# Optimization experiments

Measured on AMD Instinct MI355X. Metric: run time of the kernel, lower is better.

Reference implementation:

```python
import jax, jax.numpy as jnp
import numpy as np

D_MODEL = 1024
NUM_ATOMS = 16384
TEMPERATURE = 1.0
NEG_INF = -1e9


def setup_inputs() -> dict:
    key = jax.random.key(0)
    kx, kd, km = jax.random.split(key, 3)
    x = jax.random.normal(kx, (4, 2048, D_MODEL), dtype=jnp.float32)
    # xavier_uniform for [num_atoms, d_model]
    limit = float(np.sqrt(6.0 / (NUM_ATOMS + D_MODEL)))
    dictionary = jax.random.uniform(
        kd, (NUM_ATOMS, D_MODEL), dtype=jnp.float32, minval=-limit, maxval=limit
    )
    mask = jax.random.randint(km, (4, 2048, NUM_ATOMS), 0, 2, dtype=jnp.int32)
    return {"x": x, "dictionary": dictionary, "mask": mask}


def reference(x, dictionary, mask):
    # scores: [b, s, num_atoms]
    scores = jnp.einsum("bsd,ad->bsa", x, dictionary)
    m = mask.astype(scores.dtype)
    scores = scores * m + (1.0 - m) * NEG_INF
    weights = jax.nn.softmax(scores / TEMPERATURE, axis=-1)
    reconstruction = jnp.einsum("bsa,ad->bsd", weights, dictionary)
    argmax_indices = jnp.argmax(scores, axis=-1)
    return reconstruction, argmax_indices
```

## Files before the change

### kernel.cpp

```cpp
#include <hip/hip_runtime.h>

#define NTOK   8192
#define DMODEL 1024
#define NATOM  16384

typedef _Float16 half8  __attribute__((ext_vector_type(8)));
typedef _Float16 half4_t __attribute__((ext_vector_type(4)));
typedef float    f32x4  __attribute__((ext_vector_type(4)));

#define GLOAD_LDS16(gsrc, ldst) \
  __builtin_amdgcn_global_load_lds((const __attribute__((address_space(1))) unsigned int*)(gsrc), \
                                   (__attribute__((address_space(3))) unsigned int*)(ldst), 16, 0, 0)

__global__ void cvt_f32_f16(const float* __restrict__ in, _Float16* __restrict__ out, int n4) {
  int i = blockIdx.x * 256 + threadIdx.x;
  if (i >= n4) return;
  float4 v = ((const float4*)in)[i];
  half4_t h;
  h[0] = (_Float16)v.x; h[1] = (_Float16)v.y; h[2] = (_Float16)v.z; h[3] = (_Float16)v.w;
  ((half4_t*)out)[i] = h;
}

__global__ void transpose_dict(const float* __restrict__ dict,
                               _Float16* __restrict__ Dh, _Float16* __restrict__ dT) {
  __shared__ _Float16 tile[64][68];
  int a0 = blockIdx.x * 64;
  int d0 = blockIdx.y * 64;
  int tid = threadIdx.x;
  int c = tid & 63;
  int r0 = tid >> 6;
  #pragma unroll
  for (int i = 0; i < 16; i++) {
    int r = r0 + i * 4;
    _Float16 h = (_Float16)dict[(size_t)(a0 + r) * DMODEL + d0 + c];
    tile[r][c] = h;
    Dh[(size_t)(a0 + r) * DMODEL + d0 + c] = h;
  }
  __syncthreads();
  #pragma unroll
  for (int i = 0; i < 16; i++) {
    int rd = r0 + i * 4;
    dT[(size_t)(d0 + rd) * NATOM + a0 + c] = tile[c][rd];
  }
}

__global__ void zero_lsum(float* __restrict__ lsum) {
  lsum[blockIdx.x * 256 + threadIdx.x] = 0.0f;
}

__device__ __forceinline__ void stage_ab(const _Float16* __restrict__ A,
                                         const _Float16* __restrict__ B,
                                         _Float16* As, _Float16* Bs,
                                         size_t arow0, size_t brow0, size_t ldk,
                                         int k0, int tid) {
  #pragma unroll
  for (int i = 0; i < 2; i++) {
    int L = tid + i * 256;
    int r = L >> 2, pc = L & 3;
    int c = pc ^ ((r >> 1) & 3);
    GLOAD_LDS16(A + (arow0 + r) * ldk + k0 + c * 8, As + (size_t)L * 8);
    GLOAD_LDS16(B + (brow0 + r) * ldk + k0 + c * 8, Bs + (size_t)L * 8);
  }
}

__device__ __forceinline__ void stage_item(const _Float16* __restrict__ src, int row0,
                                           int kt, int s, _Float16* dst, int tid) {
  #pragma unroll
  for (int i = 0; i < 2; i++) {
    int L2 = tid + i * 512;
    int r = L2 >> 2, q = L2 & 3;
    int c = s * 4 + (q ^ ((r >> 1) & 3));
    GLOAD_LDS16(src + (size_t)(row0 + r) * DMODEL + kt * 64 + c * 8, dst + (size_t)L2 * 8);
  }
}

__launch_bounds__(512, 2)
__global__ void score_kernel(const _Float16* __restrict__ Xh,
                             const _Float16* __restrict__ Dh,
                             const int* __restrict__ mask,
                             _Float16* __restrict__ E,
                             float* __restrict__ lsum,
                             _Float16* __restrict__ Tmax) {
  __shared__ _Float16 lds[65536];
  const int tid  = threadIdx.x;
  const int lane = tid & 63;
  const int wave = tid >> 6;
  const int wm = wave >> 2;
  const int wn = wave & 3;
  const int m0 = blockIdx.y * 256;
  const int n0 = blockIdx.x * 256;

  const int frow = lane & 15;
  const int fkc  = lane >> 4;

  f32x4 acc[8][4] = {};

  #define AOFF(B_, S_, ROW_) ((B_) * 32768 + (S_) * 8192 + (((ROW_) << 2) + (fkc ^ (((ROW_) >> 1) & 3))) * 8)
  #define BOFF(B_, S_, ROW_) ((B_) * 32768 + 16384 + (S_) * 8192 + (((ROW_) << 2) + (fkc ^ (((ROW_) >> 1) & 3))) * 8)

  stage_item(Xh, m0, 0, 0, lds,         tid);
  stage_item(Dh, n0, 0, 0, lds + 16384, tid);
  stage_item(Xh, m0, 0, 1, lds + 8192,  tid);
  stage_item(Dh, n0, 0, 1, lds + 24576, tid);
  asm volatile("s_waitcnt vmcnt(4)" ::: "memory");
  __builtin_amdgcn_s_barrier();

  const int NKT = DMODEL / 64;
  for (int kt = 0; kt < NKT; ++kt) {
    const int b  = kt & 1;
    const int nb = b ^ 1;
    const bool more = (kt + 1 < NKT);
    half8 af[4], bf[4];

    #pragma unroll
    for (int i = 0; i < 4; i++) af[i] = *(const half8*)&lds[AOFF(b, 0, wm * 128 + i * 16 + frow)];
    #pragma unroll
    for (int j = 0; j < 4; j++) bf[j] = *(const half8*)&lds[BOFF(b, 0, wn * 64 + j * 16 + frow)];
    if (more) stage_item(Xh, m0, kt + 1, 0, lds + nb * 32768, tid);
    asm volatile("s_waitcnt lgkmcnt(0)" ::: "memory");
    __builtin_amdgcn_sched_barrier(0);
    __builtin_amdgcn_s_setprio(1);
    #pragma unroll
    for (int i = 0; i < 4; i++)
      #pragma unroll
      for (int j = 0; j < 4; j++)
        acc[i][j] = __builtin_amdgcn_mfma_f32_16x16x32_f16(af[i], bf[j], acc[i][j], 0, 0, 0);
    __builtin_amdgcn_s_setprio(0);
    __builtin_amdgcn_sched_barrier(0);
    __builtin_amdgcn_s_barrier();

    #pragma unroll
    for (int i = 0; i < 4; i++) af[i] = *(const half8*)&lds[AOFF(b, 0, wm * 128 + 64 + i * 16 + frow)];
    if (more) stage_item(Dh, n0, kt + 1, 0, lds + nb * 32768 + 16384, tid);
    asm volatile("s_waitcnt lgkmcnt(0)" ::: "memory");
    __builtin_amdgcn_sched_barrier(0);
    __builtin_amdgcn_s_setprio(1);
    #pragma unroll
    for (int i = 0; i < 4; i++)
      #pragma unroll
      for (int j = 0; j < 4; j++)
        acc[4 + i][j] = __builtin_amdgcn_mfma_f32_16x16x32_f16(af[i], bf[j], acc[4 + i][j], 0, 0, 0);
    __builtin_amdgcn_s_setprio(0);
    __builtin_amdgcn_sched_barrier(0);
    if (more) asm volatile("s_waitcnt vmcnt(4)" ::: "memory");
    else      asm volatile("s_waitcnt vmcnt(0)" ::: "memory");
    __builtin_amdgcn_s_barrier();

    #pragma unroll
    for (int i = 0; i < 4; i++) af[i] = *(const half8*)&lds[AOFF(b, 1, wm * 128 + i * 16 + frow)];
    #pragma unroll
    for (int j = 0; j < 4; j++) bf[j] = *(const half8*)&lds[BOFF(b, 1, wn * 64 + j * 16 + frow)];
    if (more) stage_item(Xh, m0, kt + 1, 1, lds + nb * 32768 + 8192, tid);
    asm volatile("s_waitcnt lgkmcnt(0)" ::: "memory");
    __builtin_amdgcn_sched_barrier(0);
    __builtin_amdgcn_s_setprio(1);
    #pragma unroll
    for (int i = 0; i < 4; i++)
      #pragma unroll
      for (int j = 0; j < 4; j++)
        acc[i][j] = __builtin_amdgcn_mfma_f32_16x16x32_f16(af[i], bf[j], acc[i][j], 0, 0, 0);
    __builtin_amdgcn_s_setprio(0);
    __builtin_amdgcn_sched_barrier(0);
    __builtin_amdgcn_s_barrier();

    #pragma unroll
    for (int i = 0; i < 4; i++) af[i] = *(const half8*)&lds[AOFF(b, 1, wm * 128 + 64 + i * 16 + frow)];
    if (more) stage_item(Dh, n0, kt + 1, 1, lds + nb * 32768 + 24576, tid);
    asm volatile("s_waitcnt lgkmcnt(0)" ::: "memory");
    __builtin_amdgcn_sched_barrier(0);
    __builtin_amdgcn_s_setprio(1);
    #pragma unroll
    for (int i = 0; i < 4; i++)
      #pragma unroll
      for (int j = 0; j < 4; j++)
        acc[4 + i][j] = __builtin_amdgcn_mfma_f32_16x16x32_f16(af[i], bf[j], acc[4 + i][j], 0, 0, 0);
    __builtin_amdgcn_s_setprio(0);
    __builtin_amdgcn_sched_barrier(0);
    if (more) asm volatile("s_waitcnt vmcnt(4)" ::: "memory");
    __builtin_amdgcn_s_barrier();
  }
  #undef AOFF
  #undef BOFF

  const int cr = (lane >> 4) * 4;
  const int cc = lane & 15;
  #pragma unroll
  for (int h = 0; h < 2; h++) {
    if ((wn >> 1) == h) {
      #pragma unroll
      for (int i = 0; i < 8; i++) {
        #pragma unroll
        for (int j = 0; j < 4; j++) {
          #pragma unroll
          for (int r = 0; r < 4; r++) {
            int lr = wm * 128 + i * 16 + cr + r;
            int lc = (wn & 1) * 64 + j * 16 + cc;
            lds[lr * 136 + lc] = (_Float16)__expf(acc[i][j][r]);
          }
        }
      }
    }
    __builtin_amdgcn_s_barrier();
    #pragma unroll
    for (int i = 0; i < 8; i++) {
      int chunk = i * 512 + tid;
      int r  = chunk >> 4;
      int c8 = (chunk & 15) * 8;
      half8 v = *(const half8*)&lds[r * 136 + c8];
      const int* mp = &mask[(size_t)(m0 + r) * NATOM + n0 + h * 128 + c8];
      int4 k0 = *(const int4*)mp;
      int4 k1 = *(const int4*)(mp + 4);
      half8 e;
      e[0] = k0.x ? v[0] : (_Float16)0.0f;
      e[1] = k0.y ? v[1] : (_Float16)0.0f;
      e[2] = k0.z ? v[2] : (_Float16)0.0f;
      e[3] = k0.w ? v[3] : (_Float16)0.0f;
      e[4] = k1.x ? v[4] : (_Float16)0.0f;
      e[5] = k1.y ? v[5] : (_Float16)0.0f;
      e[6] = k1.z ? v[6] : (_Float16)0.0f;
      e[7] = k1.w ? v[7] : (_Float16)0.0f;
      *(half8*)&E[(size_t)(m0 + r) * NATOM + n0 + h * 128 + c8] = e;
      float s = 0.0f, m = 0.0f;
      #pragma unroll
      for (int j = 0; j < 8; j++) { float f = (float)e[j]; s += f; m = fmaxf(m, f); }
      s += __shfl_xor(s, 1, 64); m = fmaxf(m, __shfl_xor(m, 1, 64));
      s += __shfl_xor(s, 2, 64); m = fmaxf(m, __shfl_xor(m, 2, 64));
      s += __shfl_xor(s, 4, 64); m = fmaxf(m, __shfl_xor(m, 4, 64));
      s += __shfl_xor(s, 8, 64); m = fmaxf(m, __shfl_xor(m, 8, 64));
      if ((tid & 15) == 0) {
        atomicAdd(&lsum[m0 + r], s);
        Tmax[(size_t)(m0 + r) * 128 + blockIdx.x * 2 + h] = (_Float16)m;
      }
    }
    __builtin_amdgcn_s_barrier();
  }
}

__global__ void scan_lite(const _Float16* __restrict__ E,
                          const _Float16* __restrict__ Tmax,
                          const float* __restrict__ x,
                          const float* __restrict__ dict,
                          float* __restrict__ argout) {
  const int wv   = threadIdx.x >> 6;
  const int lane = threadIdx.x & 63;
  const int t = blockIdx.x * 4 + wv;

  __shared__ int    cnt[4];
  __shared__ int    cand[4][32];
  __shared__ double csc[4][32];
  if (lane == 0) cnt[wv] = 0;

  const _Float16* tm = Tmax + (size_t)t * 128;
  float m0 = (float)tm[lane];
  float m1 = (float)tm[64 + lane];
  float mx = fmaxf(m0, m1);
  #pragma unroll
  for (int off = 32; off > 0; off >>= 1) mx = fmaxf(mx, __shfl_xor(mx, off, 64));

  if (mx > 0.0f) {
    float thr = 0.98f * mx;
    unsigned long long q0 = __ballot(m0 >= thr);
    unsigned long long q1 = __ballot(m1 >= thr);
    while (q0 | q1) {
      int tile;
      if (q0) { tile = __ffsll(q0) - 1; q0 &= q0 - 1; }
      else    { tile = 64 + __ffsll(q1) - 1; q1 &= q1 - 1; }
      const _Float16* ep = E + (size_t)t * NATOM + tile * 128;
      float e0 = (float)ep[lane], e1 = (float)ep[64 + lane];
      if (e0 >= thr) { int p = atomicAdd(&cnt[wv], 1); if (p < 32) cand[wv][p] = tile * 128 + lane; }
      if (e1 >= thr) { int p = atomicAdd(&cnt[wv], 1); if (p < 32) cand[wv][p] = tile * 128 + 64 + lane; }
    }
  }
  int nc = min(cnt[wv], 32);
  const float* xr = x + (size_t)t * DMODEL;
  for (int c = 0; c < nc; c++) {
    const float* dr = dict + (size_t)cand[wv][c] * DMODEL;
    double a = 0.0;
    #pragma unroll
    for (int i = 0; i < 16; i++) {
      int d = lane + i * 64;
      a += (double)xr[d] * (double)dr[d];
    }
    #pragma unroll
    for (int off = 32; off > 0; off >>= 1) a += __shfl_down(a, off, 64);
    if (lane == 0) csc[wv][c] = a;
  }
  if (lane == 0) {
    int best = 0;
    if (nc > 0) {
      double bs = -1e300;
      best = NATOM;
      for (int c = 0; c < nc; c++)
        if (csc[wv][c] > bs || (csc[wv][c] == bs && cand[wv][c] < best)) { bs = csc[wv][c]; best = cand[wv][c]; }
    }
    argout[t] = (float)best;
  }
}

__launch_bounds__(256, 2)
__global__ void recon_kernel(const _Float16* __restrict__ E,
                             const _Float16* __restrict__ DT,
                             const float* __restrict__ lsum,
                             float* __restrict__ out) {
  __shared__ _Float16 lds[32768];
  const int tid  = threadIdx.x;
  const int lane = tid & 63;
  const int wave = tid >> 6;
  const int wm = wave >> 1, wn = wave & 1;
  const int swz = (blockIdx.x & 7) * 64 + (blockIdx.x >> 3);
  const int n0 = (swz & 7) * 128;
  const int m0 = (swz >> 3) * 128;

  const int frow = lane & 15;
  const int fkc  = lane >> 4;

  f32x4 acc[4][4] = {};

  stage_ab(E, DT, lds,         lds + 4096,  m0, n0, NATOM, 0,  tid);
  stage_ab(E, DT, lds + 8192,  lds + 12288, m0, n0, NATOM, 32, tid);
  stage_ab(E, DT, lds + 16384, lds + 20480, m0, n0, NATOM, 64, tid);

  for (int t = 0; t < 512; ++t) {
    if (t < 510)       asm volatile("s_waitcnt vmcnt(8)" ::: "memory");
    else if (t == 510) asm volatile("s_waitcnt vmcnt(4)" ::: "memory");
    else               asm volatile("s_waitcnt vmcnt(0)" ::: "memory");
    __builtin_amdgcn_s_barrier();
    __builtin_amdgcn_sched_barrier(0);
    const _Float16* As = lds + (t & 3) * 8192;
    const _Float16* Bs = As + 4096;
    half8 af[4], bf[4];
    #pragma unroll
    for (int i = 0; i < 4; i++) {
      int ar = wm * 64 + i * 16 + frow;
      int br = wn * 64 + i * 16 + frow;
      af[i] = *(const half8*)&As[ar * 32 + ((fkc ^ ((ar >> 1) & 3)) << 3)];
      bf[i] = *(const half8*)&Bs[br * 32 + ((fkc ^ ((br >> 1) & 3)) << 3)];
    }
    if (t + 3 < 512) {
      int b = (t + 3) & 3;
      stage_ab(E, DT, lds + b * 8192, lds + b * 8192 + 4096, m0, n0, NATOM, (t + 3) * 32, tid);
    }
    __builtin_amdgcn_s_setprio(1);
    #pragma unroll
    for (int i = 0; i < 4; i++)
      #pragma unroll
      for (int j = 0; j < 4; j++)
        acc[i][j] = __builtin_amdgcn_mfma_f32_16x16x32_f16(af[i], bf[j], acc[i][j], 0, 0, 0);
    __builtin_amdgcn_s_setprio(0);
    __builtin_amdgcn_sched_barrier(0);
  }

  const int cr = (lane >> 4) * 4;
  const int cc = lane & 15;
  #pragma unroll
  for (int i = 0; i < 4; i++) {
    #pragma unroll
    for (int r = 0; r < 4; r++) {
      int lr = wm * 64 + i * 16 + cr + r;
      float sc = 1.0f / lsum[m0 + lr];
      #pragma unroll
      for (int j = 0; j < 4; j++) {
        int lc = wn * 64 + j * 16 + cc;
        out[(size_t)(m0 + lr) * DMODEL + (n0 + lc)] = acc[i][j][r] * sc;
      }
    }
  }
}

extern "C" void kernel_launch(void* const* d_in, const int* in_sizes, int n_in,
                              void* d_out, int out_size, void* d_ws, size_t ws_size,
                              hipStream_t stream) {
  const float* x    = (const float*)d_in[0];
  const float* dict = (const float*)d_in[1];
  const int*   mask = (const int*)d_in[2];
  float* recon  = (float*)d_out;
  float* argout = recon + (size_t)NTOK * DMODEL;

  char* w = (char*)d_ws;
  _Float16* Xh = (_Float16*)(w);
  _Float16* Dh = (_Float16*)(w + (size_t)16  * 1024 * 1024);
  _Float16* DT = (_Float16*)(w + (size_t)48  * 1024 * 1024);
  _Float16* E  = (_Float16*)(w + (size_t)80  * 1024 * 1024);
  float*  lsum = (float*)  (w + (size_t)336 * 1024 * 1024);
  _Float16* Tmax = (_Float16*)d_out;

  cvt_f32_f16<<<dim3(NTOK * DMODEL / 4 / 256), 256, 0, stream>>>(x, Xh, NTOK * DMODEL / 4);
  transpose_dict<<<dim3(NATOM / 64, DMODEL / 64), 256, 0, stream>>>(dict, Dh, DT);
  zero_lsum<<<dim3(NTOK / 256), 256, 0, stream>>>(lsum);
  score_kernel<<<dim3(NATOM / 256, NTOK / 256), 512, 0, stream>>>(Xh, Dh, mask, E, lsum, Tmax);
  scan_lite<<<dim3(NTOK / 4), 256, 0, stream>>>(E, Tmax, x, dict, argout);
  recon_kernel<<<dim3(512), 256, 0, stream>>>(E, DT, lsum, recon);
}
```

Measured before the change: 1.406 ms.

## Retile reconstruction GEMM to 256x128 blocks with 512 threads and double-buffered K=64 stages

The reconstruction GEMM moves from 128x128 tiles with 256 threads and a 4-deep K=32 ring to 256x128 tiles with 512 threads (8 waves) and double-buffered K=64 stages split into sub-steps. The A and B loads for the next stage are interleaved between MFMA groups. Block indices are remapped so each XCD handles a contiguous set of M tiles, which improves L2 reuse of E. This launches 256 blocks instead of 512, which is about one block per CU, and adds more barriers per K step.

Measured after the change: 1.361 ms. 1.03x faster.

```diff
diff --git a/kernel.cpp b/kernel.cpp
--- a/kernel.cpp
+++ b/kernel.cpp
@@ -48,21 +48,6 @@
   lsum[blockIdx.x * 256 + threadIdx.x] = 0.0f;
 }
 
-__device__ __forceinline__ void stage_ab(const _Float16* __restrict__ A,
-                                         const _Float16* __restrict__ B,
-                                         _Float16* As, _Float16* Bs,
-                                         size_t arow0, size_t brow0, size_t ldk,
-                                         int k0, int tid) {
-  #pragma unroll
-  for (int i = 0; i < 2; i++) {
-    int L = tid + i * 256;
-    int r = L >> 2, pc = L & 3;
-    int c = pc ^ ((r >> 1) & 3);
-    GLOAD_LDS16(A + (arow0 + r) * ldk + k0 + c * 8, As + (size_t)L * 8);
-    GLOAD_LDS16(B + (brow0 + r) * ldk + k0 + c * 8, Bs + (size_t)L * 8);
-  }
-}
-
 __device__ __forceinline__ void stage_item(const _Float16* __restrict__ src, int row0,
                                            int kt, int s, _Float16* dst, int tid) {
   #pragma unroll
@@ -72,6 +57,24 @@
     int c = s * 4 + (q ^ ((r >> 1) & 3));
     GLOAD_LDS16(src + (size_t)(row0 + r) * DMODEL + kt * 64 + c * 8, dst + (size_t)L2 * 8);
   }
+}
+
+__device__ __forceinline__ void rstage256(const _Float16* __restrict__ src, int row0,
+                                          size_t ldk, int k0, int s, _Float16* dst, int tid) {
+  #pragma unroll
+  for (int i = 0; i < 2; i++) {
+    int L2 = tid + i * 512;
+    int r = L2 >> 2, q = L2 & 3;
+    int c = s * 4 + (q ^ ((r >> 1) & 3));
+    GLOAD_LDS16(src + (size_t)(row0 + r) * ldk + k0 + c * 8, dst + (size_t)L2 * 8);
+  }
+}
+__device__ __forceinline__ void rstage128(const _Float16* __restrict__ src, int row0,
+                                          size_t ldk, int k0, int s, _Float16* dst, int tid) {
+  int L = tid;
+  int r = L >> 2, q = L & 3;
+  int c = s * 4 + (q ^ ((r >> 1) & 3));
+  GLOAD_LDS16(src + (size_t)(row0 + r) * ldk + k0 + c * 8, dst + (size_t)L * 8);
 }
 
 __launch_bounds__(512, 2)
@@ -297,71 +300,131 @@
   }
 }
 
-__launch_bounds__(256, 2)
+__launch_bounds__(512, 2)
 __global__ void recon_kernel(const _Float16* __restrict__ E,
                              const _Float16* __restrict__ DT,
                              const float* __restrict__ lsum,
                              float* __restrict__ out) {
-  __shared__ _Float16 lds[32768];
+  __shared__ _Float16 lds[49152];
   const int tid  = threadIdx.x;
   const int lane = tid & 63;
   const int wave = tid >> 6;
-  const int wm = wave >> 1, wn = wave & 1;
-  const int swz = (blockIdx.x & 7) * 64 + (blockIdx.x >> 3);
-  const int n0 = (swz & 7) * 128;
-  const int m0 = (swz >> 3) * 128;
+  const int wm = wave >> 2;
+  const int wn = wave & 3;
+  const int bid = blockIdx.x;
+  const int xcd = bid & 7;
+  const int idx = bid >> 3;
+  const int mt  = xcd * 4 + (idx & 3);
+  const int nt  = idx >> 2;
+  const int m0 = mt * 256;
+  const int n0 = nt * 128;
 
   const int frow = lane & 15;
   const int fkc  = lane >> 4;
 
-  f32x4 acc[4][4] = {};
-
-  stage_ab(E, DT, lds,         lds + 4096,  m0, n0, NATOM, 0,  tid);
-  stage_ab(E, DT, lds + 8192,  lds + 12288, m0, n0, NATOM, 32, tid);
-  stage_ab(E, DT, lds + 16384, lds + 20480, m0, n0, NATOM, 64, tid);
-
-  for (int t = 0; t < 512; ++t) {
-    if (t < 510)       asm volatile("s_waitcnt vmcnt(8)" ::: "memory");
-    else if (t == 510) asm volatile("s_waitcnt vmcnt(4)" ::: "memory");
-    else               asm volatile("s_waitcnt vmcnt(0)" ::: "memory");
-    __builtin_amdgcn_s_barrier();
-    __builtin_amdgcn_sched_barrier(0);
-    const _Float16* As = lds + (t & 3) * 8192;
-    const _Float16* Bs = As + 4096;
-    half8 af[4], bf[4];
-    #pragma unroll
-    for (int i = 0; i < 4; i++) {
-      int ar = wm * 64 + i * 16 + frow;
-      int br = wn * 64 + i * 16 + frow;
-      af[i] = *(const half8*)&As[ar * 32 + ((fkc ^ ((ar >> 1) & 3)) << 3)];
-      bf[i] = *(const half8*)&Bs[br * 32 + ((fkc ^ ((br >> 1) & 3)) << 3)];
-    }
-    if (t + 3 < 512) {
-      int b = (t + 3) & 3;
-      stage_ab(E, DT, lds + b * 8192, lds + b * 8192 + 4096, m0, n0, NATOM, (t + 3) * 32, tid);
-    }
-    __builtin_amdgcn_s_setprio(1);
-    #pragma unroll
-    for (int i = 0; i < 4; i++)
-      #pragma unroll
-      for (int j = 0; j < 4; j++)
+  f32x4 acc[8][2] = {};
+
+  #define RAOFF(B_, S_, ROW_) ((B_) * 24576 + (S_) * 8192 + (((ROW_) << 2) + (fkc ^ (((ROW_) >> 1) & 3))) * 8)
+  #define RBOFF(B_, S_, ROW_) ((B_) * 24576 + 16384 + (S_) * 4096 + (((ROW_) << 2) + (fkc ^ (((ROW_) >> 1) & 3))) * 8)
+
+  rstage256(E,  m0, NATOM, 0, 0, lds,         tid);
+  rstage128(DT, n0, NATOM, 0, 0, lds + 16384, tid);
+  rstage256(E,  m0, NATOM, 0, 1, lds + 8192,  tid);
+  rstage128(DT, n0, NATOM, 0, 1, lds + 20480, tid);
+  asm volatile("s_waitcnt vmcnt(3)" ::: "memory");
+  __builtin_amdgcn_s_barrier();
+
+  const int NKT = NATOM / 64;
+  for (int kt = 0; kt < NKT; ++kt) {
+    const int b  = kt & 1;
+    const int nb = b ^ 1;
+    const bool more = (kt + 1 < NKT);
+    const int k1 = (kt + 1) * 64;
+    half8 af[4], bf[2];
+
+    #pragma unroll
+    for (int i = 0; i < 4; i++) af[i] = *(const half8*)&lds[RAOFF(b, 0, wm * 128 + i * 16 + frow)];
+    #pragma unroll
+    for (int j = 0; j < 2; j++) bf[j] = *(const half8*)&lds[RBOFF(b, 0, wn * 32 + j * 16 + frow)];
+    if (more) rstage256(E, m0, NATOM, k1, 0, lds + nb * 24576, tid);
+    asm volatile("s_waitcnt lgkmcnt(0)" ::: "memory");
+    __builtin_amdgcn_sched_barrier(0);
+    __builtin_amdgcn_s_setprio(1);
+    #pragma unroll
+    for (int i = 0; i < 4; i++)
+      #pragma unroll
+      for (int j = 0; j < 2; j++)
         acc[i][j] = __builtin_amdgcn_mfma_f32_16x16x32_f16(af[i], bf[j], acc[i][j], 0, 0, 0);
     __builtin_amdgcn_s_setprio(0);
     __builtin_amdgcn_sched_barrier(0);
-  }
+    __builtin_amdgcn_s_barrier();
+
+    #pragma unroll
+    for (int i = 0; i < 4; i++) af[i] = *(const half8*)&lds[RAOFF(b, 0, wm * 128 + 64 + i * 16 + frow)];
+    if (more) rstage128(DT, n0, NATOM, k1, 0, lds + nb * 24576 + 16384, tid);
+    asm volatile("s_waitcnt lgkmcnt(0)" ::: "memory");
+    __builtin_amdgcn_sched_barrier(0);
+    __builtin_amdgcn_s_setprio(1);
+    #pragma unroll
+    for (int i = 0; i < 4; i++)
+      #pragma unroll
+      for (int j = 0; j < 2; j++)
+        acc[4 + i][j] = __builtin_amdgcn_mfma_f32_16x16x32_f16(af[i], bf[j], acc[4 + i][j], 0, 0, 0);
+    __builtin_amdgcn_s_setprio(0);
+    __builtin_amdgcn_sched_barrier(0);
+    if (more) asm volatile("s_waitcnt vmcnt(3)" ::: "memory");
+    else      asm volatile("s_waitcnt vmcnt(0)" ::: "memory");
+    __builtin_amdgcn_s_barrier();
+
+    #pragma unroll
+    for (int i = 0; i < 4; i++) af[i] = *(const half8*)&lds[RAOFF(b, 1, wm * 128 + i * 16 + frow)];
+    #pragma unroll
+    for (int j = 0; j < 2; j++) bf[j] = *(const half8*)&lds[RBOFF(b, 1, wn * 32 + j * 16 + frow)];
+    if (more) rstage256(E, m0, NATOM, k1, 1, lds + nb * 24576 + 8192, tid);
+    asm volatile("s_waitcnt lgkmcnt(0)" ::: "memory");
+    __builtin_amdgcn_sched_barrier(0);
+    __builtin_amdgcn_s_setprio(1);
+    #pragma unroll
+    for (int i = 0; i < 4; i++)
+      #pragma unroll
+      for (int j = 0; j < 2; j++)
+        acc[i][j] = __builtin_amdgcn_mfma_f32_16x16x32_f16(af[i], bf[j], acc[i][j], 0, 0, 0);
+    __builtin_amdgcn_s_setprio(0);
+    __builtin_amdgcn_sched_barrier(0);
+    __builtin_amdgcn_s_barrier();
+
+    #pragma unroll
+    for (int i = 0; i < 4; i++) af[i] = *(const half8*)&lds[RAOFF(b, 1, wm * 128 + 64 + i * 16 + frow)];
+    if (more) rstage128(DT, n0, NATOM, k1, 1, lds + nb * 24576 + 20480, tid);
+    asm volatile("s_waitcnt lgkmcnt(0)" ::: "memory");
+    __builtin_amdgcn_sched_barrier(0);
+    __builtin_amdgcn_s_setprio(1);
+    #pragma unroll
+    for (int i = 0; i < 4; i++)
+      #pragma unroll
+      for (int j = 0; j < 2; j++)
+        acc[4 + i][j] = __builtin_amdgcn_mfma_f32_16x16x32_f16(af[i], bf[j], acc[4 + i][j], 0, 0, 0);
+    __builtin_amdgcn_s_setprio(0);
+    __builtin_amdgcn_sched_barrier(0);
+    if (more) asm volatile("s_waitcnt vmcnt(3)" ::: "memory");
+    __builtin_amdgcn_s_barrier();
+  }
+  #undef RAOFF
+  #undef RBOFF
 
   const int cr = (lane >> 4) * 4;
   const int cc = lane & 15;
   #pragma unroll
-  for (int i = 0; i < 4; i++) {
+  for (int a = 0; a < 8; a++) {
+    int rowbase = wm * 128 + (a >> 2) * 64 + (a & 3) * 16 + cr;
     #pragma unroll
     for (int r = 0; r < 4; r++) {
-      int lr = wm * 64 + i * 16 + cr + r;
+      int lr = rowbase + r;
       float sc = 1.0f / lsum[m0 + lr];
       #pragma unroll
-      for (int j = 0; j < 4; j++) {
-        int lc = wn * 64 + j * 16 + cc;
-        out[(size_t)(m0 + lr) * DMODEL + (n0 + lc)] = acc[i][j][r] * sc;
+      for (int j = 0; j < 2; j++) {
+        int lc = wn * 32 + j * 16 + cc;
+        out[(size_t)(m0 + lr) * DMODEL + (n0 + lc)] = acc[a][j][r] * sc;
       }
     }
   }
@@ -389,5 +452,5 @@
   zero_lsum<<<dim3(NTOK / 256), 256, 0, stream>>>(lsum);
   score_kernel<<<dim3(NATOM / 256, NTOK / 256), 512, 0, stream>>>(Xh, Dh, mask, E, lsum, Tmax);
   scan_lite<<<dim3(NTOK / 4), 256, 0, stream>>>(E, Tmax, x, dict, argout);
-  recon_kernel<<<dim3(512), 256, 0, stream>>>(E, DT, lsum, recon);
-}
+  recon_kernel<<<dim3(256), 512, 0, stream>>>(E, DT, lsum, recon);
+}
```
